# Kernel tuning notes

Measured on AMD Instinct MI355X. Metric: run time of the kernel, lower is better.

## Reference

```python
import math
import jax, jax.numpy as jnp
from jax import lax
import numpy as np

L, B, S, H, N = 2, 1, 2048, 1024, 16
HN = H // N
EPS = 1e-5
SIGMA = 0.02
OUT_STD = SIGMA / math.sqrt(2.0 * L)


def gelu(x):
    # OpenAI tanh-approx gelu, matching gelu_impl
    return 0.5 * x * (1.0 + jnp.tanh(0.7978845608028654 * x * (1.0 + 0.044715 * x * x)))


def layer_norm(x, g, b):
    mu = jnp.mean(x, axis=-1, keepdims=True)
    var = jnp.mean(jnp.square(x - mu), axis=-1, keepdims=True)
    return (x - mu) / jnp.sqrt(var + EPS) * g + b


def setup_inputs() -> dict:
    key = jax.random.key(0)
    ks = jax.random.split(key, 8)
    x = jax.random.normal(ks[0], (B, S, H), dtype=jnp.float32)
    ltor_mask = jnp.tril(jnp.ones((S, S), dtype=jnp.float32))[None, None]  # [1,1,S,S]
    return {
        "hidden_states": x,
        "ltor_mask": ltor_mask,
        "ln1_g": jnp.ones((L, H), jnp.float32),
        "ln1_b": jnp.zeros((L, H), jnp.float32),
        "qkv_w": jax.random.normal(ks[1], (L, H, 3 * H), jnp.float32) * SIGMA,
        "qkv_b": jnp.zeros((L, 3 * H), jnp.float32),
        "dense_w": jax.random.normal(ks[2], (L, H, H), jnp.float32) * OUT_STD,
        "dense_b": jnp.zeros((L, H), jnp.float32),
        "ln2_g": jnp.ones((L, H), jnp.float32),
        "ln2_b": jnp.zeros((L, H), jnp.float32),
        "fc_w": jax.random.normal(ks[3], (L, H, 4 * H), jnp.float32) * SIGMA,
        "fc_b": jnp.zeros((L, 4 * H), jnp.float32),
        "proj_w": jax.random.normal(ks[4], (L, 4 * H, H), jnp.float32) * OUT_STD,
        "proj_b": jnp.zeros((L, H), jnp.float32),
        "lnf_g": jnp.ones((H,), jnp.float32),
        "lnf_b": jnp.zeros((H,), jnp.float32),
    }


def _transformer(hidden_states, ltor_mask, ln1_g, ln1_b, qkv_w, qkv_b, dense_w, dense_b,
                 ln2_g, ln2_b, fc_w, fc_b, proj_w, proj_b, lnf_g, lnf_b):
    scale = 1.0 / math.sqrt(HN)

    def step(h, p):
        g1, b1, qw, qb, dw, db, g2, b2, fw, fb, pw, pb = p
        y = layer_norm(h, g1, b1)
        qkv = y @ qw + qb                       # [B,S,3H]
        q, k, v = jnp.split(qkv, 3, axis=-1)
        # [B,S,H] -> [B,N,S,HN]
        q = q.reshape(B, S, N, HN).transpose(0, 2, 1, 3)
        k = k.reshape(B, S, N, HN).transpose(0, 2, 1, 3)
        v = v.reshape(B, S, N, HN).transpose(0, 2, 1, 3)
        scores = jnp.einsum('bnqd,bnkd->bnqk', q, k) * scale
        scores = scores * ltor_mask - 10000.0 * (1.0 - ltor_mask)
        probs = jax.nn.softmax(scores, axis=-1)
        ctx = jnp.einsum('bnqk,bnkd->bnqd', probs, v)
        ctx = ctx.transpose(0, 2, 1, 3).reshape(B, S, H)
        attn_out = ctx @ dw + db
        h2 = h + attn_out
        y2 = layer_norm(h2, g2, b2)
        mlp_out = gelu(y2 @ fw + fb) @ pw + pb
        return h2 + mlp_out, None

    params = (ln1_g, ln1_b, qkv_w, qkv_b, dense_w, dense_b,
              ln2_g, ln2_b, fc_w, fc_b, proj_w, proj_b)
    h, _ = lax.scan(step, hidden_states, params)
    return layer_norm(h, lnf_g, lnf_b)


def reference(hidden_states, ltor_mask, ln1_g, ln1_b, qkv_w, qkv_b, dense_w, dense_b,
              ln2_g, ln2_b, fc_w, fc_b, proj_w, proj_b, lnf_g, lnf_b):
    return _transformer(hidden_states, ltor_mask, ln1_g, ln1_b, qkv_w, qkv_b,
                        dense_w, dense_b, ln2_g, ln2_b, fc_w, fc_b,
                        proj_w, proj_b, lnf_g, lnf_b)
```

## Files before the change

### kernel.cpp

```cpp
#include <hip/hip_runtime.h>
#include <hip/hip_bf16.h>
#include <cstdint>
#include <cstddef>

typedef __bf16 bf16;
typedef __attribute__((ext_vector_type(4))) __bf16 bf16x4;
typedef __attribute__((ext_vector_type(8))) __bf16 bf16x8;
typedef __attribute__((ext_vector_type(4))) float floatx4;

__device__ __forceinline__ void gload16(const bf16* g, bf16* l) {
    __builtin_amdgcn_global_load_lds(
        (const __attribute__((address_space(1))) void*)g,
        (__attribute__((address_space(3))) void*)l, 16, 0, 0);
}

__global__ __launch_bounds__(256) void ln_first(const float* __restrict__ x,
                                                float* __restrict__ h,
                                                const float* __restrict__ g,
                                                const float* __restrict__ b,
                                                bf16* __restrict__ y) {
    __shared__ float red[8];
    const int row = blockIdx.x, tid = threadIdx.x;
    const size_t off = (size_t)row * 1024 + tid * 4;
    const float4 v = *(const float4*)(x + off);
    *(float4*)(h + off) = v;
    float s = v.x + v.y + v.z + v.w;
#pragma unroll
    for (int o = 32; o > 0; o >>= 1) s += __shfl_xor(s, o);
    if ((tid & 63) == 0) red[tid >> 6] = s;
    __syncthreads();
    const float mean = (red[0] + red[1] + red[2] + red[3]) * (1.f / 1024.f);
    const float d[4] = {v.x - mean, v.y - mean, v.z - mean, v.w - mean};
    float q = d[0] * d[0] + d[1] * d[1] + d[2] * d[2] + d[3] * d[3];
#pragma unroll
    for (int o = 32; o > 0; o >>= 1) q += __shfl_xor(q, o);
    if ((tid & 63) == 0) red[4 + (tid >> 6)] = q;
    __syncthreads();
    const float var = (red[4] + red[5] + red[6] + red[7]) * (1.f / 1024.f);
    const float rstd = rsqrtf(var + 1e-5f);
    const int base = tid * 4;
#pragma unroll
    for (int i = 0; i < 4; i++)
        y[off + i] = (bf16)(d[i] * rstd * g[base + i] + b[base + i]);
}

template <typename OutT, int KS>
__global__ __launch_bounds__(256) void reduce_ln(const bf16* __restrict__ part,
                                                 const float* __restrict__ bias,
                                                 float* __restrict__ h,
                                                 const float* __restrict__ g,
                                                 const float* __restrict__ b,
                                                 OutT* __restrict__ y) {
    __shared__ float red[8];
    const int row = blockIdx.x, tid = threadIdx.x;
    const int base = tid * 4;
    const size_t off = (size_t)row * 1024 + base;
    const float4 hv = *(const float4*)(h + off);
    const float4 bv = *(const float4*)(bias + base);
    float a[4] = {hv.x + bv.x, hv.y + bv.y, hv.z + bv.z, hv.w + bv.w};
#pragma unroll
    for (int z = 0; z < KS; z++) {
        bf16x4 pv = *(const bf16x4*)(part + (size_t)z * (2048 * 1024) + off);
#pragma unroll
        for (int i = 0; i < 4; i++) a[i] += (float)pv[i];
    }
    *(float4*)(h + off) = (float4){a[0], a[1], a[2], a[3]};
    float s = a[0] + a[1] + a[2] + a[3];
#pragma unroll
    for (int o = 32; o > 0; o >>= 1) s += __shfl_xor(s, o);
    if ((tid & 63) == 0) red[tid >> 6] = s;
    __syncthreads();
    const float mean = (red[0] + red[1] + red[2] + red[3]) * (1.f / 1024.f);
    const float d[4] = {a[0] - mean, a[1] - mean, a[2] - mean, a[3] - mean};
    float q = d[0] * d[0] + d[1] * d[1] + d[2] * d[2] + d[3] * d[3];
#pragma unroll
    for (int o = 32; o > 0; o >>= 1) q += __shfl_xor(q, o);
    if ((tid & 63) == 0) red[4 + (tid >> 6)] = q;
    __syncthreads();
    const float var = (red[4] + red[5] + red[6] + red[7]) * (1.f / 1024.f);
    const float rstd = rsqrtf(var + 1e-5f);
#pragma unroll
    for (int i = 0; i < 4; i++)
        y[off + i] = (OutT)(d[i] * rstd * g[base + i] + b[base + i]);
}

__global__ __launch_bounds__(256) void transpose_all(const float* __restrict__ qkv_w,
                                                     const float* __restrict__ dense_w,
                                                     const float* __restrict__ fc_w,
                                                     const float* __restrict__ proj_w,
                                                     bf16* __restrict__ wT) {
    __shared__ float T[64][65];
    int b = blockIdx.x;
    const int layer = (b >= 3072) ? 1 : 0;
    b -= layer * 3072;
    const float* src; bf16* dst; int K, N, kx, ny;
    bf16* wl = wT + (size_t)layer * 12582912;
    if (b < 768)       { src = qkv_w  + (size_t)layer * 1024 * 3072; dst = wl;            K = 1024; N = 3072; kx = b & 15; ny = b >> 4; }
    else if (b < 1024) { b -= 768;  src = dense_w + (size_t)layer * 1024 * 1024; dst = wl + 3145728; K = 1024; N = 1024; kx = b & 15; ny = b >> 4; }
    else if (b < 2048) { b -= 1024; src = fc_w    + (size_t)layer * 1024 * 4096; dst = wl + 4194304; K = 1024; N = 4096; kx = b & 15; ny = b >> 4; }
    else               { b -= 2048; src = proj_w  + (size_t)layer * 4096 * 1024; dst = wl + 8388608; K = 4096; N = 1024; kx = b & 63; ny = b >> 6; }
    const int k0 = kx * 64, n0 = ny * 64;
    {
        const int r = threadIdx.x >> 4;
        const int c4 = (threadIdx.x & 15) * 4;
#pragma unroll
        for (int j = 0; j < 4; j++) {
            float4 v = *(const float4*)&src[(size_t)(k0 + r + j * 16) * N + n0 + c4];
            T[r + j * 16][c4 + 0] = v.x; T[r + j * 16][c4 + 1] = v.y;
            T[r + j * 16][c4 + 2] = v.z; T[r + j * 16][c4 + 3] = v.w;
        }
    }
    __syncthreads();
    {
        const int rn = threadIdx.x >> 3;
        const int c8 = (threadIdx.x & 7) * 8;
#pragma unroll
        for (int j = 0; j < 2; j++) {
            bf16x8 v;
#pragma unroll
            for (int i = 0; i < 8; i++) v[i] = (bf16)T[c8 + i][rn + j * 32];
            *(bf16x8*)&dst[(size_t)(n0 + rn + j * 32) * K + k0 + c8] = v;
        }
    }
}

template <int MODE>
__global__ __launch_bounds__(256) void gemm_bt64(const bf16* __restrict__ A,
                                                 const bf16* __restrict__ BT,
                                                 const float* __restrict__ bias,
                                                 bf16* __restrict__ outb,
                                                 int M, int N, int K) {
    __shared__ bf16 As[64 * 64];
    __shared__ bf16 Bs[128 * 64];
    const int tid = threadIdx.x;
    const int w = tid >> 6, lane = tid & 63;
    const int quad = lane >> 4, l16 = lane & 15;
    const int wm = w >> 1, wn = w & 1;
    const int m0 = blockIdx.x * 64, n0 = blockIdx.y * 128;
    const int kchunk = K / gridDim.z;
    const int kbeg = blockIdx.z * kchunk;

    const int srow = lane >> 3;
    const int scol = ((lane & 7) ^ srow) * 8;
    const bf16* ga = A + (size_t)(m0 + w * 16 + srow) * K + kbeg + scol;
    const bf16* gb = BT + (size_t)(n0 + w * 32 + srow) * K + kbeg + scol;
    bf16* la = As + (w * 16) * 64;
    bf16* lb = Bs + (w * 32) * 64;

    floatx4 acc[2][4];
#pragma unroll
    for (int i = 0; i < 2; i++)
#pragma unroll
        for (int j = 0; j < 4; j++) acc[i][j] = (floatx4){0.f, 0.f, 0.f, 0.f};

#pragma unroll
    for (int s = 0; s < 2; s++) gload16(ga + (size_t)(s * 8) * K, la + s * 8 * 64);
#pragma unroll
    for (int s = 0; s < 4; s++) gload16(gb + (size_t)(s * 8) * K, lb + s * 8 * 64);

    const int xq = (l16 & 7) * 8;

    for (int kk = 0; kk < kchunk; kk += 64) {
        __syncthreads();
        bf16x8 af[2][2], bfr[2][4];
#pragma unroll
        for (int ks = 0; ks < 2; ks++) {
            const int colz = (ks * 32 + quad * 8) ^ xq;
#pragma unroll
            for (int i = 0; i < 2; i++)
                af[ks][i]  = *(const bf16x8*)&As[(wm * 32 + i * 16 + l16) * 64 + colz];
#pragma unroll
            for (int i = 0; i < 4; i++)
                bfr[ks][i] = *(const bf16x8*)&Bs[(wn * 64 + i * 16 + l16) * 64 + colz];
        }
        __syncthreads();
        if (kk + 64 < kchunk) {
#pragma unroll
            for (int s = 0; s < 2; s++) gload16(ga + (size_t)(s * 8) * K + kk + 64, la + s * 8 * 64);
#pragma unroll
            for (int s = 0; s < 4; s++) gload16(gb + (size_t)(s * 8) * K + kk + 64, lb + s * 8 * 64);
        }
#pragma unroll
        for (int ks = 0; ks < 2; ks++)
#pragma unroll
            for (int ms = 0; ms < 2; ms++)
#pragma unroll
                for (int ns = 0; ns < 4; ns++)
                    acc[ms][ns] = __builtin_amdgcn_mfma_f32_16x16x32_bf16(af[ks][ms], bfr[ks][ns],
                                                                          acc[ms][ns], 0, 0, 0);
    }

    bf16* pout = (MODE == 2) ? (outb + (size_t)blockIdx.z * M * N) : outb;
#pragma unroll
    for (int ms = 0; ms < 2; ms++) {
#pragma unroll
        for (int ns = 0; ns < 4; ns++) {
            const int row = m0 + wm * 32 + ms * 16 + quad * 4;
            const int col = n0 + wn * 64 + ns * 16 + l16;
            const float bv = (MODE == 2) ? 0.f : bias[col];
#pragma unroll
            for (int i = 0; i < 4; i++) {
                float v = acc[ms][ns][i] + bv;
                size_t idx = (size_t)(row + i) * N + col;
                if (MODE == 1) {
                    float t = 0.7978845608028654f * v * (1.f + 0.044715f * v * v);
                    pout[idx] = (bf16)(0.5f * v * (1.f + tanhf(t)));
                } else {
                    pout[idx] = (bf16)v;
                }
            }
        }
    }
}

__global__ __launch_bounds__(256) void attn_mfma(const bf16* __restrict__ qkv,
                                                 bf16* __restrict__ ctx) {
    __shared__ bf16 Ks[64][68];
    __shared__ bf16 Vt[64][72];
    __shared__ bf16 QP[64][68];
    const int tid = threadIdx.x;
    const int w = tid >> 6, lane = tid & 63;
    const int quad = lane >> 4, l16 = lane & 15;
    const int head = blockIdx.y;
    const int qt = 31 - blockIdx.x;
    const int q0 = qt * 64;
    const int rowg = w * 16 + quad * 4;
    const int r = tid >> 2;
    const int c = (tid & 3) * 16;
    const float SC = 0.18033688011111827f;

    {
        const bf16* pq = qkv + (size_t)(q0 + r) * 3072 + head * 64 + c;
        bf16x8 a0 = *(const bf16x8*)pq, a1 = *(const bf16x8*)(pq + 8);
        bf16x8 s0, s1;
#pragma unroll
        for (int i = 0; i < 8; i++) {
            s0[i] = (bf16)((float)a0[i] * SC); s1[i] = (bf16)((float)a1[i] * SC);
        }
        *(bf16x8*)&QP[r][c] = s0; *(bf16x8*)&QP[r][c + 8] = s1;
    }
    const bf16x8 aq0 = *(const bf16x8*)&QP[w * 16 + l16][quad * 8];
    const bf16x8 aq1 = *(const bf16x8*)&QP[w * 16 + l16][32 + quad * 8];

    float ls[4] = {0.f, 0.f, 0.f, 0.f};
    floatx4 o[4];
#pragma unroll
    for (int d = 0; d < 4; d++) o[d] = (floatx4){0.f, 0.f, 0.f, 0.f};

    const int nt = qt + 1;
    bf16x8 kr0, kr1, vr0, vr1;
    {
        const bf16* kp = qkv + (size_t)r * 3072 + 1024 + head * 64 + c;
        kr0 = *(const bf16x8*)kp; kr1 = *(const bf16x8*)(kp + 8);
        const bf16* vp = qkv + (size_t)lane * 3072 + 2048 + head * 64 + w * 16;
        vr0 = *(const bf16x8*)vp; vr1 = *(const bf16x8*)(vp + 8);
    }

    for (int t = 0; t < nt; t++) {
        __syncthreads();
        *(bf16x8*)&Ks[r][c] = kr0;
        *(bf16x8*)&Ks[r][c + 8] = kr1;
#pragma unroll
        for (int i = 0; i < 8; i++) {
            Vt[w * 16 + i][lane] = vr0[i];
            Vt[w * 16 + 8 + i][lane] = vr1[i];
        }
        __syncthreads();
        if (t + 1 < nt) {
            const size_t kb = (size_t)(t + 1) * 64;
            const bf16* kp = qkv + (kb + r) * 3072 + 1024 + head * 64 + c;
            kr0 = *(const bf16x8*)kp; kr1 = *(const bf16x8*)(kp + 8);
            const bf16* vp = qkv + (kb + lane) * 3072 + 2048 + head * 64 + w * 16;
            vr0 = *(const bf16x8*)vp; vr1 = *(const bf16x8*)(vp + 8);
        }

        floatx4 s4[4];
#pragma unroll
        for (int n = 0; n < 4; n++) s4[n] = (floatx4){0.f, 0.f, 0.f, 0.f};
#pragma unroll
        for (int n = 0; n < 4; n++) {
            bf16x8 bk0 = *(const bf16x8*)&Ks[n * 16 + l16][quad * 8];
            bf16x8 bk1 = *(const bf16x8*)&Ks[n * 16 + l16][32 + quad * 8];
            s4[n] = __builtin_amdgcn_mfma_f32_16x16x32_bf16(aq0, bk0, s4[n], 0, 0, 0);
            s4[n] = __builtin_amdgcn_mfma_f32_16x16x32_bf16(aq1, bk1, s4[n], 0, 0, 0);
        }

        {
            float p[4][4];
            if (t == nt - 1) {
#pragma unroll
                for (int i = 0; i < 4; i++)
#pragma unroll
                    for (int n = 0; n < 4; n++)
                        p[n][i] = (n * 16 + l16 > rowg + i) ? 0.f
                                  : __builtin_amdgcn_exp2f(s4[n][i]);
            } else {
#pragma unroll
                for (int i = 0; i < 4; i++)
#pragma unroll
                    for (int n = 0; n < 4; n++)
                        p[n][i] = __builtin_amdgcn_exp2f(s4[n][i]);
            }
#pragma unroll
            for (int i = 0; i < 4; i++)
#pragma unroll
                for (int n = 0; n < 4; n++) ls[i] += p[n][i];
#pragma unroll
            for (int n = 0; n < 4; n++)
#pragma unroll
                for (int i = 0; i < 4; i++)
                    QP[rowg + i][n * 16 + l16] = (bf16)p[n][i];
        }

        {
            bf16x8 ap0 = *(const bf16x8*)&QP[w * 16 + l16][quad * 8];
            bf16x8 ap1 = *(const bf16x8*)&QP[w * 16 + l16][32 + quad * 8];
#pragma unroll
            for (int d = 0; d < 4; d++) {
                bf16x8 bv0 = *(const bf16x8*)&Vt[d * 16 + l16][quad * 8];
                bf16x8 bv1 = *(const bf16x8*)&Vt[d * 16 + l16][32 + quad * 8];
                o[d] = __builtin_amdgcn_mfma_f32_16x16x32_bf16(ap0, bv0, o[d], 0, 0, 0);
                o[d] = __builtin_amdgcn_mfma_f32_16x16x32_bf16(ap1, bv1, o[d], 0, 0, 0);
            }
        }
    }

#pragma unroll
    for (int i = 0; i < 4; i++) {
#pragma unroll
        for (int msk = 1; msk < 16; msk <<= 1)
            ls[i] += __shfl_xor(ls[i], msk);
    }
#pragma unroll
    for (int i = 0; i < 4; i++) {
        const float rl = 1.f / ls[i];
        const size_t rb = (size_t)(q0 + rowg + i) * 1024 + head * 64;
#pragma unroll
        for (int d = 0; d < 4; d++)
            ctx[rb + d * 16 + l16] = (bf16)(o[d][i] * rl);
    }
}

extern "C" void kernel_launch(void* const* d_in, const int* in_sizes, int n_in,
                              void* d_out, int out_size, void* d_ws, size_t ws_size,
                              hipStream_t stream) {
    const float* hidden  = (const float*)d_in[0];
    const float* ln1_g   = (const float*)d_in[2];
    const float* ln1_b   = (const float*)d_in[3];
    const float* qkv_w   = (const float*)d_in[4];
    const float* qkv_b   = (const float*)d_in[5];
    const float* dense_w = (const float*)d_in[6];
    const float* dense_b = (const float*)d_in[7];
    const float* ln2_g   = (const float*)d_in[8];
    const float* ln2_b   = (const float*)d_in[9];
    const float* fc_w    = (const float*)d_in[10];
    const float* fc_b    = (const float*)d_in[11];
    const float* proj_w  = (const float*)d_in[12];
    const float* proj_b  = (const float*)d_in[13];
    const float* lnf_g   = (const float*)d_in[14];
    const float* lnf_b   = (const float*)d_in[15];

    char* ws = (char*)d_ws;
    float* h    = (float*)(ws);
    bf16* y     = (bf16*)(ws + 8u   * 1024 * 1024);
    bf16* qkvb  = (bf16*)(ws + 12u  * 1024 * 1024);
    bf16* ctx   = (bf16*)(ws + 24u  * 1024 * 1024);
    bf16* mlp   = (bf16*)(ws + 12u  * 1024 * 1024);
    bf16* part  = (bf16*)(ws + 36u  * 1024 * 1024);
    bf16* wT    = (bf16*)(ws + 52u  * 1024 * 1024);

    const size_t LW = 12582912;

    transpose_all<<<6144, 256, 0, stream>>>(qkv_w, dense_w, fc_w, proj_w, wT);
    ln_first<<<2048, 256, 0, stream>>>(hidden, h, ln1_g, ln1_b, y);

    for (int l = 0; l < 2; l++) {
        bf16* wTq = wT + (size_t)l * LW;
        bf16* wTd = wTq + 3145728;
        bf16* wTf = wTq + 4194304;
        bf16* wTp = wTq + 8388608;

        gemm_bt64<0><<<dim3(32, 24, 1), 256, 0, stream>>>(y, wTq, qkv_b + l * 3072, qkvb, 2048, 3072, 1024);
        attn_mfma<<<dim3(32, 16), 256, 0, stream>>>(qkvb, ctx);

        gemm_bt64<2><<<dim3(32, 8, 4), 256, 0, stream>>>(ctx, wTd, nullptr, part, 2048, 1024, 1024);
        reduce_ln<bf16, 4><<<2048, 256, 0, stream>>>(part, dense_b + l * 1024, h,
                                                     ln2_g + l * 1024, ln2_b + l * 1024, y);

        gemm_bt64<1><<<dim3(32, 32, 1), 256, 0, stream>>>(y, wTf, fc_b + l * 4096, mlp, 2048, 4096, 1024);
        gemm_bt64<2><<<dim3(32, 8, 4), 256, 0, stream>>>(mlp, wTp, nullptr, part, 2048, 1024, 4096);
        if (l == 0) {
            reduce_ln<bf16, 4><<<2048, 256, 0, stream>>>(part, proj_b, h,
                                                         ln1_g + 1024, ln1_b + 1024, y);
        } else {
            reduce_ln<float, 4><<<2048, 256, 0, stream>>>(part, proj_b + 1024, h,
                                                          lnf_g, lnf_b, (float*)d_out);
        }
    }
}
```

Baseline: 458.0 us.

## Pair causal attention query tiles per block to balance triangular work

Each attention block now has 512 threads holding two query tiles, qta and 31-qta, and every K/V tile loaded into shared memory is shared by both. The grid is halved so each block carries a balanced amount of causal work, and loading K/V once for two tiles cuts redundant global loads. The cost is larger blocks with more shared memory, and the short-tile waves sit idle after their diagonal while they still take part in the barriers.

```diff
diff --git a/kernel.cpp b/kernel.cpp
--- a/kernel.cpp
+++ b/kernel.cpp
@@ -213,81 +213,90 @@
     }
 }
 
-__global__ __launch_bounds__(256) void attn_mfma(const bf16* __restrict__ qkv,
+__global__ __launch_bounds__(512) void attn_mfma(const bf16* __restrict__ qkv,
                                                  bf16* __restrict__ ctx) {
     __shared__ bf16 Ks[64][68];
     __shared__ bf16 Vt[64][72];
-    __shared__ bf16 QP[64][68];
+    __shared__ bf16 QPa[64][68];
+    __shared__ bf16 QPb[64][68];
     const int tid = threadIdx.x;
     const int w = tid >> 6, lane = tid & 63;
     const int quad = lane >> 4, l16 = lane & 15;
+    const int w4 = w & 3;
+    const int grp = w >> 2;
     const int head = blockIdx.y;
-    const int qt = 31 - blockIdx.x;
-    const int q0 = qt * 64;
-    const int rowg = w * 16 + quad * 4;
-    const int r = tid >> 2;
-    const int c = (tid & 3) * 16;
+    const int qta = blockIdx.x;
+    const int qtb = 31 - qta;
+    const int qmyt = grp ? qtb : qta;
+    const int qmy0 = qmyt * 64;
+    const int rowg = w4 * 16 + quad * 4;
     const float SC = 0.18033688011111827f;
 
+    bf16 (* const QPown)[68] = grp ? QPb : QPa;
+
     {
-        const bf16* pq = qkv + (size_t)(q0 + r) * 3072 + head * 64 + c;
+        const int tt = tid & 255;
+        const int r = tt >> 2;
+        const int c = (tt & 3) * 16;
+        const bf16* pq = qkv + (size_t)(qmy0 + r) * 3072 + head * 64 + c;
         bf16x8 a0 = *(const bf16x8*)pq, a1 = *(const bf16x8*)(pq + 8);
         bf16x8 s0, s1;
 #pragma unroll
         for (int i = 0; i < 8; i++) {
             s0[i] = (bf16)((float)a0[i] * SC); s1[i] = (bf16)((float)a1[i] * SC);
         }
-        *(bf16x8*)&QP[r][c] = s0; *(bf16x8*)&QP[r][c + 8] = s1;
-    }
-    const bf16x8 aq0 = *(const bf16x8*)&QP[w * 16 + l16][quad * 8];
-    const bf16x8 aq1 = *(const bf16x8*)&QP[w * 16 + l16][32 + quad * 8];
+        *(bf16x8*)&QPown[r][c] = s0; *(bf16x8*)&QPown[r][c + 8] = s1;
+    }
+    const bf16x8 aq0 = *(const bf16x8*)&QPown[w4 * 16 + l16][quad * 8];
+    const bf16x8 aq1 = *(const bf16x8*)&QPown[w4 * 16 + l16][32 + quad * 8];
 
     float ls[4] = {0.f, 0.f, 0.f, 0.f};
     floatx4 o[4];
 #pragma unroll
     for (int d = 0; d < 4; d++) o[d] = (floatx4){0.f, 0.f, 0.f, 0.f};
 
-    const int nt = qt + 1;
-    bf16x8 kr0, kr1, vr0, vr1;
+    const int krow = tid >> 3;
+    const int kcol = (tid & 7) * 8;
+    const int vcol = tid & 63;
+    const int vd = (tid >> 6) * 8;
+
+    const int nt = qtb + 1;
+    bf16x8 kr, vr;
     {
-        const bf16* kp = qkv + (size_t)r * 3072 + 1024 + head * 64 + c;
-        kr0 = *(const bf16x8*)kp; kr1 = *(const bf16x8*)(kp + 8);
-        const bf16* vp = qkv + (size_t)lane * 3072 + 2048 + head * 64 + w * 16;
-        vr0 = *(const bf16x8*)vp; vr1 = *(const bf16x8*)(vp + 8);
+        const bf16* kp = qkv + (size_t)krow * 3072 + 1024 + head * 64 + kcol;
+        kr = *(const bf16x8*)kp;
+        const bf16* vp = qkv + (size_t)vcol * 3072 + 2048 + head * 64 + vd;
+        vr = *(const bf16x8*)vp;
     }
 
     for (int t = 0; t < nt; t++) {
         __syncthreads();
-        *(bf16x8*)&Ks[r][c] = kr0;
-        *(bf16x8*)&Ks[r][c + 8] = kr1;
-#pragma unroll
-        for (int i = 0; i < 8; i++) {
-            Vt[w * 16 + i][lane] = vr0[i];
-            Vt[w * 16 + 8 + i][lane] = vr1[i];
-        }
+        *(bf16x8*)&Ks[krow][kcol] = kr;
+#pragma unroll
+        for (int i = 0; i < 8; i++) Vt[vd + i][vcol] = vr[i];
         __syncthreads();
         if (t + 1 < nt) {
             const size_t kb = (size_t)(t + 1) * 64;
-            const bf16* kp = qkv + (kb + r) * 3072 + 1024 + head * 64 + c;
-            kr0 = *(const bf16x8*)kp; kr1 = *(const bf16x8*)(kp + 8);
-            const bf16* vp = qkv + (kb + lane) * 3072 + 2048 + head * 64 + w * 16;
-            vr0 = *(const bf16x8*)vp; vr1 = *(const bf16x8*)(vp + 8);
-        }
-
-        floatx4 s4[4];
-#pragma unroll
-        for (int n = 0; n < 4; n++) s4[n] = (floatx4){0.f, 0.f, 0.f, 0.f};
-#pragma unroll
-        for (int n = 0; n < 4; n++) {
-            bf16x8 bk0 = *(const bf16x8*)&Ks[n * 16 + l16][quad * 8];
-            bf16x8 bk1 = *(const bf16x8*)&Ks[n * 16 + l16][32 + quad * 8];
-            s4[n] = __builtin_amdgcn_mfma_f32_16x16x32_bf16(aq0, bk0, s4[n], 0, 0, 0);
-            s4[n] = __builtin_amdgcn_mfma_f32_16x16x32_bf16(aq1, bk1, s4[n], 0, 0, 0);
-        }
-
-        {
+            const bf16* kp = qkv + (kb + krow) * 3072 + 1024 + head * 64 + kcol;
+            kr = *(const bf16x8*)kp;
+            const bf16* vp = qkv + (kb + vcol) * 3072 + 2048 + head * 64 + vd;
+            vr = *(const bf16x8*)vp;
+        }
+        const bool act = grp ? true : (t <= qta);
+        if (act) {
+            floatx4 s4[4];
+#pragma unroll
+            for (int n = 0; n < 4; n++) s4[n] = (floatx4){0.f, 0.f, 0.f, 0.f};
+#pragma unroll
+            for (int n = 0; n < 4; n++) {
+                bf16x8 bk0 = *(const bf16x8*)&Ks[n * 16 + l16][quad * 8];
+                bf16x8 bk1 = *(const bf16x8*)&Ks[n * 16 + l16][32 + quad * 8];
+                s4[n] = __builtin_amdgcn_mfma_f32_16x16x32_bf16(aq0, bk0, s4[n], 0, 0, 0);
+                s4[n] = __builtin_amdgcn_mfma_f32_16x16x32_bf16(aq1, bk1, s4[n], 0, 0, 0);
+            }
+
             float p[4][4];
-            if (t == nt - 1) {
+            if (t == qmyt) {
 #pragma unroll
                 for (int i = 0; i < 4; i++)
 #pragma unroll
@@ -309,12 +318,10 @@
             for (int n = 0; n < 4; n++)
 #pragma unroll
                 for (int i = 0; i < 4; i++)
-                    QP[rowg + i][n * 16 + l16] = (bf16)p[n][i];
-        }
-
-        {
-            bf16x8 ap0 = *(const bf16x8*)&QP[w * 16 + l16][quad * 8];
-            bf16x8 ap1 = *(const bf16x8*)&QP[w * 16 + l16][32 + quad * 8];
+                    QPown[rowg + i][n * 16 + l16] = (bf16)p[n][i];
+
+            bf16x8 ap0 = *(const bf16x8*)&QPown[w4 * 16 + l16][quad * 8];
+            bf16x8 ap1 = *(const bf16x8*)&QPown[w4 * 16 + l16][32 + quad * 8];
 #pragma unroll
             for (int d = 0; d < 4; d++) {
                 bf16x8 bv0 = *(const bf16x8*)&Vt[d * 16 + l16][quad * 8];
@@ -334,7 +341,7 @@
 #pragma unroll
     for (int i = 0; i < 4; i++) {
         const float rl = 1.f / ls[i];
-        const size_t rb = (size_t)(q0 + rowg + i) * 1024 + head * 64;
+        const size_t rb = (size_t)(qmy0 + rowg + i) * 1024 + head * 64;
 #pragma unroll
         for (int d = 0; d < 4; d++)
             ctx[rb + d * 16 + l16] = (bf16)(o[d][i] * rl);
@@ -381,7 +388,7 @@
         bf16* wTp = wTq + 8388608;
 
         gemm_bt64<0><<<dim3(32, 24, 1), 256, 0, stream>>>(y, wTq, qkv_b + l * 3072, qkvb, 2048, 3072, 1024);
-        attn_mfma<<<dim3(32, 16), 256, 0, stream>>>(qkvb, ctx);
+        attn_mfma<<<dim3(16, 16), 512, 0, stream>>>(qkvb, ctx);
 
         gemm_bt64<2><<<dim3(32, 8, 4), 256, 0, stream>>>(ctx, wTd, nullptr, part, 2048, 1024, 1024);
         reduce_ln<bf16, 4><<<2048, 256, 0, stream>>>(part, dense_b + l * 1024, h,
```

After: 451.1 us. About the same (-1.5%).
